# Kernel optimization log

Measured on AMD Instinct MI355X. Metric: run time of the kernel, lower is better.

The kernel has to match this reference:

```python
import jax, jax.numpy as jnp
import numpy as np

N_NODES = 20000
N_EDGES = 640000


def graph_conv(x, src, dst, W, b, n_nodes):
    """DGL GraphConv with norm='both': D_in^{-1/2} A D_out^{-1/2} X W + b."""
    ones = jnp.ones(src.shape[0], dtype=x.dtype)
    deg_out = jnp.maximum(jax.ops.segment_sum(ones, src, num_segments=n_nodes), 1.0)
    deg_in = jnp.maximum(jax.ops.segment_sum(ones, dst, num_segments=n_nodes), 1.0)
    xs = x * (deg_out ** -0.5)[:, None]          # scale src features
    agg = jax.ops.segment_sum(xs[src], dst, num_segments=n_nodes)  # [N, d]
    agg = agg * (deg_in ** -0.5)[:, None]
    return agg @ W + b


def setup_inputs() -> dict:
    key = jax.random.key(0)
    ks = jax.random.split(key, 10)
    d = 256
    scale = 1.0 / np.sqrt(d)
    return {
        "x": jax.random.normal(ks[0], (N_NODES, d), dtype=jnp.float32),
        "side_src": jax.random.randint(ks[1], (N_EDGES,), 0, N_NODES),
        "side_dst": jax.random.randint(ks[2], (N_EDGES,), 0, N_NODES),
        "upd_src": jax.random.randint(ks[3], (N_EDGES,), 0, N_NODES),
        "upd_dst": jax.random.randint(ks[4], (N_EDGES,), 0, N_NODES),
        "W1_side": jax.random.normal(ks[5], (d, d), dtype=jnp.float32) * scale,
        "b1_side": jnp.zeros((d,), dtype=jnp.float32),
        "W1_upd": jax.random.normal(ks[6], (d, d), dtype=jnp.float32) * scale,
        "b1_upd": jnp.zeros((d,), dtype=jnp.float32),
        "W2_side": jax.random.normal(ks[7], (d, d), dtype=jnp.float32) * scale,
        "b2_side": jnp.zeros((d,), dtype=jnp.float32),
        "W2_upd": jax.random.normal(ks[8], (d, d), dtype=jnp.float32) * scale,
        "b2_upd": jnp.zeros((d,), dtype=jnp.float32),
    }


def reference(x, side_src, side_dst, upd_src, upd_dst,
              W1_side, b1_side, W1_upd, b1_upd,
              W2_side, b2_side, W2_upd, b2_upd):
    n = x.shape[0]
    # layer 1: HeteroGraphConv with aggregate='sum' over relations, then relu
    h = (graph_conv(x, side_src, side_dst, W1_side, b1_side, n)
         + graph_conv(x, upd_src, upd_dst, W1_upd, b1_upd, n))
    h = jax.nn.relu(h)
    # layer 2
    out = (graph_conv(h, side_src, side_dst, W2_side, b2_side, n)
           + graph_conv(h, upd_src, upd_dst, W2_upd, b2_upd, n))
    return out
```

## Files before the change

### kernel.cpp

```cpp
#include <hip/hip_runtime.h>

typedef __attribute__((ext_vector_type(8))) short short8;
typedef __attribute__((ext_vector_type(4))) float f32x4;

#define SCHUNK 2048
#define MAXN   20480
#define NSLICE 8
#define NPB    40

__device__ inline unsigned short f2bf(float v) {
    unsigned u = __float_as_uint(v);
    u += 0x7FFFu + ((u >> 16) & 1u);
    return (unsigned short)(u >> 16);
}
__device__ inline float bf2f(unsigned short h) {
    return __uint_as_float((unsigned)h << 16);
}

__global__ void bias_sum_kernel(const float* __restrict__ b1s, const float* __restrict__ b1u,
                                const float* __restrict__ b2s, const float* __restrict__ b2u,
                                float* __restrict__ bsum1, float* __restrict__ bsum2) {
    int i = threadIdx.x;
    bsum1[i] = b1s[i] + b1u[i];
    bsum2[i] = b2s[i] + b2u[i];
}

__global__ void wprep_kernel(const float* __restrict__ W1s, const float* __restrict__ W1u,
                             const float* __restrict__ W2s, const float* __restrict__ W2u,
                             unsigned short* __restrict__ Bpk1, unsigned short* __restrict__ Bpk2) {
    int k = blockIdx.x;
    int nn = threadIdx.x;
    int layer = blockIdx.y;
    const float* Ws = layer ? W2s : W1s;
    const float* Wu = layer ? W2u : W1u;
    float w = (k < 256) ? Ws[k * 256 + nn] : Wu[(k - 256) * 256 + nn];
    unsigned short hi = f2bf(w);
    unsigned short lo = f2bf(w - bf2f(hi));
    unsigned short* B = layer ? Bpk2 : Bpk1;
    size_t frag = ((size_t)(nn >> 4) * 16 + (k >> 5)) * 2;
    size_t addr = frag * 512 + ((nn & 15) + ((k >> 3) & 3) * 16) * 8 + (k & 7);
    B[addr] = hi;
    B[addr + 512] = lo;
}

__global__ __launch_bounds__(256) void hist_kernel(
    const int* __restrict__ sS, const int* __restrict__ dS,
    const int* __restrict__ sU, const int* __restrict__ dU,
    int Es, int Eu, int n, int nblk, unsigned int* __restrict__ histG) {
    __shared__ unsigned int h[MAXN];
    const int rel = blockIdx.y;
    const int* src = rel ? sU : sS;
    const int* dst = rel ? dU : dS;
    int E = rel ? Eu : Es;
    int b = blockIdx.x;
    int chunk = (E + nblk - 1) / nblk;
    int beg = b * chunk;
    int end = min(E, beg + chunk);
    for (int i = threadIdx.x; i < n; i += 256) h[i] = 0u;
    __syncthreads();
    for (int i = beg + threadIdx.x; i < end; i += 256) {
        atomicAdd(&h[src[i]], 1u);
        atomicAdd(&h[dst[i]], 0x10000u);
    }
    __syncthreads();
    unsigned int* out = histG + ((size_t)rel * nblk + b) * n;
    for (int i = threadIdx.x; i < n; i += 256) out[i] = h[i];
}

__global__ void totals_kernel(const unsigned int* __restrict__ histG, int n, int nblk,
                              float* __restrict__ sOutS, float* __restrict__ sInS,
                              float* __restrict__ sOutU, float* __restrict__ sInU,
                              int* __restrict__ degInS, int* __restrict__ degInU) {
    const int rel = blockIdx.y;
    int i = blockIdx.x * 256 + threadIdx.x;
    if (i >= n) return;
    const unsigned int* hg = histG + (size_t)rel * nblk * n + i;
    unsigned int lo = 0, hi = 0;
    int b = 0;
    for (; b + 8 <= nblk; b += 8) {
        unsigned v0 = hg[(size_t)(b + 0) * n];
        unsigned v1 = hg[(size_t)(b + 1) * n];
        unsigned v2 = hg[(size_t)(b + 2) * n];
        unsigned v3 = hg[(size_t)(b + 3) * n];
        unsigned v4 = hg[(size_t)(b + 4) * n];
        unsigned v5 = hg[(size_t)(b + 5) * n];
        unsigned v6 = hg[(size_t)(b + 6) * n];
        unsigned v7 = hg[(size_t)(b + 7) * n];
        lo += (v0 & 0xFFFFu) + (v1 & 0xFFFFu) + (v2 & 0xFFFFu) + (v3 & 0xFFFFu)
            + (v4 & 0xFFFFu) + (v5 & 0xFFFFu) + (v6 & 0xFFFFu) + (v7 & 0xFFFFu);
        hi += (v0 >> 16) + (v1 >> 16) + (v2 >> 16) + (v3 >> 16)
            + (v4 >> 16) + (v5 >> 16) + (v6 >> 16) + (v7 >> 16);
    }
    for (; b < nblk; ++b) {
        unsigned v = hg[(size_t)b * n];
        lo += v & 0xFFFFu;
        hi += v >> 16;
    }
    float so = rsqrtf((float)(lo > 1u ? lo : 1u));
    float si = rsqrtf((float)(hi > 1u ? hi : 1u));
    if (rel) { sOutU[i] = so; sInU[i] = si; degInU[i] = (int)hi; }
    else     { sOutS[i] = so; sInS[i] = si; degInS[i] = (int)hi; }
}

__global__ __launch_bounds__(256) void scan_part_kernel(const int* __restrict__ degA,
                                                        const int* __restrict__ degB,
                                                        int n, int NB, int* __restrict__ bsum) {
    const int rel = blockIdx.y;
    const int* deg = rel ? degB : degA;
    int t = threadIdx.x;
    int base = blockIdx.x * SCHUNK + t * 8;
    int s = 0;
    if (base + 8 <= n) {
        int4 a = *(const int4*)(deg + base);
        int4 b = *(const int4*)(deg + base + 4);
        s = a.x + a.y + a.z + a.w + b.x + b.y + b.z + b.w;
    } else {
        for (int i = 0; i < 8; ++i)
            if (base + i < n) s += deg[base + i];
    }
    __shared__ int sm[256];
    sm[t] = s;
    __syncthreads();
    for (int off = 128; off > 0; off >>= 1) {
        if (t < off) sm[t] += sm[t + off];
        __syncthreads();
    }
    if (t == 0) bsum[rel * NB + blockIdx.x] = sm[0];
}

__global__ void scan_mid_kernel(int* __restrict__ bsum, int NB,
                                int* __restrict__ rpA, int* __restrict__ rpB, int n) {
    int t = threadIdx.x;
    if (t >= 2) return;
    int* bs = bsum + t * NB;
    int run = 0;
    for (int i = 0; i < NB; ++i) {
        int v = bs[i];
        bs[i] = run;
        run += v;
    }
    int* rp = t ? rpB : rpA;
    rp[n] = run;
}

__global__ __launch_bounds__(256) void scan_final_kernel(const int* __restrict__ degA,
                                                         const int* __restrict__ degB,
                                                         const int* __restrict__ bsum,
                                                         int n, int NB,
                                                         int* __restrict__ rpA,
                                                         int* __restrict__ rpB) {
    const int rel = blockIdx.y;
    const int* deg = rel ? degB : degA;
    int* rp = rel ? rpB : rpA;
    int t = threadIdx.x;
    int base = blockIdx.x * SCHUNK + t * 8;
    int v[8];
    if (base + 8 <= n) {
        int4 a = *(const int4*)(deg + base);
        int4 b = *(const int4*)(deg + base + 4);
        v[0] = a.x; v[1] = a.y; v[2] = a.z; v[3] = a.w;
        v[4] = b.x; v[5] = b.y; v[6] = b.z; v[7] = b.w;
    } else {
        for (int i = 0; i < 8; ++i) v[i] = (base + i < n) ? deg[base + i] : 0;
    }
    int s = 0;
    #pragma unroll
    for (int i = 0; i < 8; ++i) s += v[i];
    __shared__ int sm[256];
    sm[t] = s;
    __syncthreads();
    #pragma unroll
    for (int off = 1; off < 256; off <<= 1) {
        int y = (t >= off) ? sm[t - off] : 0;
        __syncthreads();
        sm[t] += y;
        __syncthreads();
    }
    int run = bsum[rel * NB + blockIdx.x] + sm[t] - s;
    #pragma unroll
    for (int i = 0; i < 8; ++i) {
        if (base + i < n) rp[base + i] = run;
        run += v[i];
    }
}

__global__ void offsets_kernel(const unsigned int* __restrict__ histG,
                               const int* __restrict__ rpS, const int* __restrict__ rpU,
                               int n, int nblk, int* __restrict__ offsG) {
    const int rel = blockIdx.y;
    int i = blockIdx.x * 256 + threadIdx.x;
    if (i >= n) return;
    const unsigned int* hg = histG + (size_t)rel * nblk * n + i;
    int* og = offsG + (size_t)rel * nblk * n + i;
    int run = (rel ? rpU : rpS)[i];
    int b = 0;
    for (; b + 8 <= nblk; b += 8) {
        unsigned v0 = hg[(size_t)(b + 0) * n];
        unsigned v1 = hg[(size_t)(b + 1) * n];
        unsigned v2 = hg[(size_t)(b + 2) * n];
        unsigned v3 = hg[(size_t)(b + 3) * n];
        unsigned v4 = hg[(size_t)(b + 4) * n];
        unsigned v5 = hg[(size_t)(b + 5) * n];
        unsigned v6 = hg[(size_t)(b + 6) * n];
        unsigned v7 = hg[(size_t)(b + 7) * n];
        og[(size_t)(b + 0) * n] = run; run += (int)(v0 >> 16);
        og[(size_t)(b + 1) * n] = run; run += (int)(v1 >> 16);
        og[(size_t)(b + 2) * n] = run; run += (int)(v2 >> 16);
        og[(size_t)(b + 3) * n] = run; run += (int)(v3 >> 16);
        og[(size_t)(b + 4) * n] = run; run += (int)(v4 >> 16);
        og[(size_t)(b + 5) * n] = run; run += (int)(v5 >> 16);
        og[(size_t)(b + 6) * n] = run; run += (int)(v6 >> 16);
        og[(size_t)(b + 7) * n] = run; run += (int)(v7 >> 16);
    }
    for (; b < nblk; ++b) {
        unsigned v = hg[(size_t)b * n];
        og[(size_t)b * n] = run;
        run += (int)(v >> 16);
    }
}

__global__ __launch_bounds__(256) void csr_scatter_kernel(
    const int* __restrict__ sS, const int* __restrict__ dS,
    const int* __restrict__ sU, const int* __restrict__ dU,
    int Es, int Eu, int n, int nblk, const int* __restrict__ offsG,
    const float* __restrict__ sOutS, const float* __restrict__ sOutU,
    int2* __restrict__ csrPS, int2* __restrict__ csrPU) {
    __shared__ int off[MAXN];
    const int rel = blockIdx.y;
    const int* src = rel ? sU : sS;
    const int* dst = rel ? dU : dS;
    const float* so = rel ? sOutU : sOutS;
    int2* csrP = rel ? csrPU : csrPS;
    int E = rel ? Eu : Es;
    int b = blockIdx.x;
    int chunk = (E + nblk - 1) / nblk;
    int beg = b * chunk;
    int end = min(E, beg + chunk);
    const int* og = offsG + ((size_t)rel * nblk + b) * n;
    for (int i = threadIdx.x; i < n; i += 256) off[i] = og[i];
    __syncthreads();
    for (int i = beg + threadIdx.x; i < end; i += 256) {
        int s = src[i];
        int pos = atomicAdd(&off[dst[i]], 1);
        csrP[pos] = make_int2(s, __float_as_int(so[s]));
    }
}

__global__ __launch_bounds__(256) void pull_slice_kernel(
    const float4* __restrict__ xin,
    const int2* __restrict__ csrPS, const int2* __restrict__ csrPU,
    const int* __restrict__ rpS, const int* __restrict__ rpU,
    const float* __restrict__ sinS, const float* __restrict__ sinU,
    unsigned short* __restrict__ aggPk, int n) {
    int bid = blockIdx.x;
    int slice = bid & (NSLICE - 1);
    int rest = bid >> 3;
    int rel = rest & 1;
    int chunk = rest >> 1;
    const int2* csrP = rel ? csrPU : csrPS;
    const int* rp = rel ? rpU : rpS;
    const float* sinv = rel ? sinU : sinS;

    int wave = threadIdx.x >> 6;
    int lane = threadIdx.x & 63;
    int sub = lane >> 3;
    int sl = lane & 7;
    int fbase = slice * 8 + sl;
    int kstepg = rel * 8 + slice;

    int start = chunk * NPB;
    int lim = min(n, start + NPB);
    for (int node = start + wave; node < lim; node += 4) {
        int beg = rp[node], end = rp[node + 1];
        float ax = 0.f, ay = 0.f, az = 0.f, aw = 0.f;
        for (int eb = beg; eb < end; eb += 64) {
            int cnt = end - eb;
            if (cnt > 64) cnt = 64;
            int myu = 0;
            float myw = 0.f;
            if (lane < cnt) {
                int2 p = csrP[eb + lane];
                myu = p.x;
                myw = __int_as_float(p.y);
            }
            int jmax = (cnt + 7) >> 3;
            int j = 0;
            for (; j + 4 <= jmax; j += 4) {
                int i0 = j * 8 + sub;
                int u0 = __shfl(myu, i0);
                int u1 = __shfl(myu, i0 + 8);
                int u2 = __shfl(myu, i0 + 16);
                int u3 = __shfl(myu, i0 + 24);
                float w0 = __shfl(myw, i0);
                float w1 = __shfl(myw, i0 + 8);
                float w2 = __shfl(myw, i0 + 16);
                float w3 = __shfl(myw, i0 + 24);
                float4 a0 = xin[(size_t)u0 * 64 + fbase];
                float4 a1 = xin[(size_t)u1 * 64 + fbase];
                float4 a2 = xin[(size_t)u2 * 64 + fbase];
                float4 a3 = xin[(size_t)u3 * 64 + fbase];
                ax += w0 * a0.x + w1 * a1.x + w2 * a2.x + w3 * a3.x;
                ay += w0 * a0.y + w1 * a1.y + w2 * a2.y + w3 * a3.y;
                az += w0 * a0.z + w1 * a1.z + w2 * a2.z + w3 * a3.z;
                aw += w0 * a0.w + w1 * a1.w + w2 * a2.w + w3 * a3.w;
            }
            for (; j < jmax; ++j) {
                int idx = j * 8 + sub;
                int u = __shfl(myu, idx);
                float w = __shfl(myw, idx);
                float4 a = xin[(size_t)u * 64 + fbase];
                ax += w * a.x; ay += w * a.y; az += w * a.z; aw += w * a.w;
            }
        }
        ax += __shfl_xor(ax, 8);  ax += __shfl_xor(ax, 16); ax += __shfl_xor(ax, 32);
        ay += __shfl_xor(ay, 8);  ay += __shfl_xor(ay, 16); ay += __shfl_xor(ay, 32);
        az += __shfl_xor(az, 8);  az += __shfl_xor(az, 16); az += __shfl_xor(az, 32);
        aw += __shfl_xor(aw, 8);  aw += __shfl_xor(aw, 16); aw += __shfl_xor(aw, 32);
        if (sub == 0) {
            float si = sinv[node];
            float vx = si * ax, vy = si * ay, vz = si * az, vw = si * aw;
            ushort4 hi4 = make_ushort4(f2bf(vx), f2bf(vy), f2bf(vz), f2bf(vw));
            ushort4 lo4 = make_ushort4(f2bf(vx - bf2f(hi4.x)), f2bf(vy - bf2f(hi4.y)),
                                       f2bf(vz - bf2f(hi4.z)), f2bf(vw - bf2f(hi4.w)));
            size_t frag = ((size_t)(node >> 4) * 16 + kstepg) * 2;
            size_t addr = frag * 512 + ((node & 15) + (sl >> 1) * 16) * 8 + (sl & 1) * 4;
            *(ushort4*)&aggPk[addr] = hi4;
            *(ushort4*)&aggPk[addr + 512] = lo4;
        }
    }
}

template <int RELU>
__global__ __launch_bounds__(512) void gemm_mfma_kernel(
    const short8* __restrict__ Apk, const short8* __restrict__ Bpk,
    const float* __restrict__ bias, float* __restrict__ C, int M) {
    __shared__ short8 lds[42][64];
    int tid = threadIdx.x;
    int lane = tid & 63;
    int wv = tid >> 6;
    int mt0 = blockIdx.x * 5;
    int m0 = blockIdx.x * 80;
    if (m0 >= M) return;
    int nt0 = wv * 2;
    int col0 = wv * 32;
    int frow = lane & 15;

    f32x4 acc[5][2];
    #pragma unroll
    for (int fr = 0; fr < 5; ++fr)
        #pragma unroll
        for (int fc = 0; fc < 2; ++fc)
            acc[fr][fc] = (f32x4){0.f, 0.f, 0.f, 0.f};

    for (int ks = 0; ks < 16; ++ks) {
        __syncthreads();
        #pragma unroll
        for (int r = 0; r < 6; ++r) {
            int s = r * 512 + tid;
            if (s < 2688) {
                int f = s >> 6, l = s & 63;
                if (f < 10) {
                    int fr = f >> 1, pl = f & 1;
                    lds[f][l] = Apk[((size_t)(mt0 + fr) * 16 + ks) * 128 + pl * 64 + l];
                } else {
                    int q = f - 10;
                    int nt = q >> 1, pl = q & 1;
                    lds[f][l] = Bpk[((size_t)nt * 16 + ks) * 128 + pl * 64 + l];
                }
            }
        }
        __syncthreads();
        short8 bh[2], bl[2];
        #pragma unroll
        for (int fc = 0; fc < 2; ++fc) {
            bh[fc] = lds[10 + (nt0 + fc) * 2 + 0][lane];
            bl[fc] = lds[10 + (nt0 + fc) * 2 + 1][lane];
        }
        #pragma unroll
        for (int fr = 0; fr < 5; ++fr) {
            short8 ah = lds[fr * 2 + 0][lane];
            short8 al = lds[fr * 2 + 1][lane];
            #pragma unroll
            for (int fc = 0; fc < 2; ++fc) {
                acc[fr][fc] = __builtin_amdgcn_mfma_f32_16x16x32_bf16(ah, bh[fc], acc[fr][fc], 0, 0, 0);
                acc[fr][fc] = __builtin_amdgcn_mfma_f32_16x16x32_bf16(al, bh[fc], acc[fr][fc], 0, 0, 0);
                acc[fr][fc] = __builtin_amdgcn_mfma_f32_16x16x32_bf16(ah, bl[fc], acc[fr][fc], 0, 0, 0);
            }
        }
    }

    #pragma unroll
    for (int fr = 0; fr < 5; ++fr)
        #pragma unroll
        for (int fc = 0; fc < 2; ++fc) {
            int c = col0 + fc * 16 + frow;
            float bc = bias[c];
            int rb = m0 + fr * 16 + (lane >> 4) * 4;
            #pragma unroll
            for (int j = 0; j < 4; ++j) {
                int r = rb + j;
                if (r < M) {
                    float v = acc[fr][fc][j] + bc;
                    if (RELU) v = fmaxf(v, 0.f);
                    C[(size_t)r * 256 + c] = v;
                }
            }
        }
}

extern "C" void kernel_launch(void* const* d_in, const int* in_sizes, int n_in,
                              void* d_out, int out_size, void* d_ws, size_t ws_size,
                              hipStream_t stream) {
    const float* x   = (const float*)d_in[0];
    const int* sS    = (const int*)d_in[1];
    const int* dS    = (const int*)d_in[2];
    const int* sU    = (const int*)d_in[3];
    const int* dU    = (const int*)d_in[4];
    const float* W1s = (const float*)d_in[5];
    const float* b1s = (const float*)d_in[6];
    const float* W1u = (const float*)d_in[7];
    const float* b1u = (const float*)d_in[8];
    const float* W2s = (const float*)d_in[9];
    const float* b2s = (const float*)d_in[10];
    const float* W2u = (const float*)d_in[11];
    const float* b2u = (const float*)d_in[12];
    float* out = (float*)d_out;

    const int n  = in_sizes[0] / 256;
    const int Es = in_sizes[1];
    const int Eu = in_sizes[3];
    const int NB = (n + SCHUNK - 1) / SCHUNK;
    const int gemmGrid = (n + 79) / 80;
    const size_t AGG_BYTES = (size_t)((n + 15) / 16 + 16) * 16 * 2 * 512 * 2;
    const size_t BPK_BYTES = (size_t)16 * 16 * 2 * 512 * 2;

    auto plan = [&](int nb) -> size_t {
        size_t t = 0;
        auto add = [&](size_t b) { t = (t + 255) & ~(size_t)255; t += b; };
        add((size_t)2 * nb * n * 4);
        add((size_t)2 * nb * n * 4);
        add((size_t)(n + 1) * 4); add((size_t)(n + 1) * 4);
        add((size_t)n * 4); add((size_t)n * 4); add((size_t)n * 4); add((size_t)n * 4);
        add((size_t)n * 4); add((size_t)n * 4);
        add(256 * 4); add(256 * 4);
        add((size_t)2 * NB * 4);
        add((size_t)Es * 8); add((size_t)Eu * 8);
        add(2 * BPK_BYTES);
        add(AGG_BYTES);
        add((size_t)n * 256 * 4);
        return t;
    };
    const int nblk = (plan(128) <= ws_size) ? 128 : 32;

    char* ws = (char*)d_ws;
    size_t off = 0;
    auto alloc = [&](size_t bytes) -> void* {
        off = (off + 255) & ~(size_t)255;
        void* p = ws + off;
        off += bytes;
        return p;
    };

    unsigned int* histG = (unsigned int*)alloc((size_t)2 * nblk * n * 4);
    int* offsG   = (int*)alloc((size_t)2 * nblk * n * 4);
    int* rpS     = (int*)alloc((size_t)(n + 1) * 4);
    int* rpU     = (int*)alloc((size_t)(n + 1) * 4);
    float* sOutS = (float*)alloc((size_t)n * 4);
    float* sInS  = (float*)alloc((size_t)n * 4);
    float* sOutU = (float*)alloc((size_t)n * 4);
    float* sInU  = (float*)alloc((size_t)n * 4);
    int* degInS  = (int*)alloc((size_t)n * 4);
    int* degInU  = (int*)alloc((size_t)n * 4);
    float* bsum1 = (float*)alloc(256 * 4);
    float* bsum2 = (float*)alloc(256 * 4);
    int* bsumBlk = (int*)alloc((size_t)2 * NB * 4);
    int2* csrPS  = (int2*)alloc((size_t)Es * 8);
    int2* csrPU  = (int2*)alloc((size_t)Eu * 8);
    unsigned short* Bpk1 = (unsigned short*)alloc(2 * BPK_BYTES);
    unsigned short* Bpk2 = Bpk1 + BPK_BYTES / 2;
    unsigned short* aggPk = (unsigned short*)alloc(AGG_BYTES);
    float* h     = (float*)alloc((size_t)n * 256 * 4);

    bias_sum_kernel<<<1, 256, 0, stream>>>(b1s, b1u, b2s, b2u, bsum1, bsum2);
    wprep_kernel<<<dim3(512, 2), 256, 0, stream>>>(W1s, W1u, W2s, W2u, Bpk1, Bpk2);
    dim3 hg(nblk, 2);
    hist_kernel<<<hg, 256, 0, stream>>>(sS, dS, sU, dU, Es, Eu, n, nblk, histG);
    dim3 tg((n + 255) / 256, 2);
    totals_kernel<<<tg, 256, 0, stream>>>(histG, n, nblk, sOutS, sInS, sOutU, sInU,
                                          degInS, degInU);
    dim3 sg(NB, 2);
    scan_part_kernel<<<sg, 256, 0, stream>>>(degInS, degInU, n, NB, bsumBlk);
    scan_mid_kernel<<<1, 64, 0, stream>>>(bsumBlk, NB, rpS, rpU, n);
    scan_final_kernel<<<sg, 256, 0, stream>>>(degInS, degInU, bsumBlk, n, NB, rpS, rpU);
    offsets_kernel<<<tg, 256, 0, stream>>>(histG, rpS, rpU, n, nblk, offsG);
    csr_scatter_kernel<<<hg, 256, 0, stream>>>(sS, dS, sU, dU, Es, Eu, n, nblk, offsG,
                                               sOutS, sOutU, csrPS, csrPU);

    int chunks = (n + NPB - 1) / NPB;
    int pullGrid = NSLICE * 2 * chunks;
    const float4* x4 = (const float4*)x;
    const float4* h4 = (const float4*)h;
    const short8* A8 = (const short8*)aggPk;
    const short8* B81 = (const short8*)Bpk1;
    const short8* B82 = (const short8*)Bpk2;

    pull_slice_kernel<<<pullGrid, 256, 0, stream>>>(x4, csrPS, csrPU, rpS, rpU,
                                                    sInS, sInU, aggPk, n);
    gemm_mfma_kernel<1><<<gemmGrid, 512, 0, stream>>>(A8, B81, bsum1, h, n);
    pull_slice_kernel<<<pullGrid, 256, 0, stream>>>(h4, csrPS, csrPU, rpS, rpU,
                                                    sInS, sInU, aggPk, n);
    gemm_mfma_kernel<0><<<gemmGrid, 512, 0, stream>>>(A8, B82, bsum2, out, n);
}
```

Measured before the change: 456.6 us.

## Prefetch next node's edges into LDS and double-buffer GEMM tiles

In the pull kernel, each wave now stages the first 64 edges of its node in LDS and prefetches the next node's row pointers and edges while the current node is being gathered. This replaces per-edge shuffles with LDS reads and hides index-load latency. The GEMM kernel switches to double-buffered LDS with register staging, so global loads for the next k-step overlap MFMA work and one barrier per step is removed. The cost is more registers and LDS per block, which may reduce occupancy.

```diff
diff --git a/kernel.cpp b/kernel.cpp
--- a/kernel.cpp
+++ b/kernel.cpp
@@ -252,6 +252,7 @@
     const int* __restrict__ rpS, const int* __restrict__ rpU,
     const float* __restrict__ sinS, const float* __restrict__ sinU,
     unsigned short* __restrict__ aggPk, int n) {
+    __shared__ int2 elds[4][64];
     int bid = blockIdx.x;
     int slice = bid & (NSLICE - 1);
     int rest = bid >> 3;
@@ -270,42 +271,67 @@
 
     int start = chunk * NPB;
     int lim = min(n, start + NPB);
-    for (int node = start + wave; node < lim; node += 4) {
-        int beg = rp[node], end = rp[node + 1];
+    int node = start + wave;
+    if (node >= lim) return;
+
+    int beg = rp[node], end = rp[node + 1];
+    {
+        int cnt = min(end - beg, 64);
+        int2 p = make_int2(0, 0);
+        if (lane < cnt) p = csrP[beg + lane];
+        elds[wave][lane] = p;
+    }
+    const int2* ebase = &elds[wave][sub];
+
+    while (node < lim) {
+        int next = node + 4;
+        int nbeg = 0, nend = 0;
+        int2 np = make_int2(0, 0);
+        if (next < lim) {
+            nbeg = rp[next];
+            nend = rp[next + 1];
+            int ncnt = min(nend - nbeg, 64);
+            if (lane < ncnt) np = csrP[nbeg + lane];
+        }
         float ax = 0.f, ay = 0.f, az = 0.f, aw = 0.f;
-        for (int eb = beg; eb < end; eb += 64) {
-            int cnt = end - eb;
-            if (cnt > 64) cnt = 64;
+        int cnt = min(end - beg, 64);
+        int jmax = (cnt + 7) >> 3;
+        int j = 0;
+        for (; j + 4 <= jmax; j += 4) {
+            int2 e0 = ebase[(j + 0) * 8];
+            int2 e1 = ebase[(j + 1) * 8];
+            int2 e2 = ebase[(j + 2) * 8];
+            int2 e3 = ebase[(j + 3) * 8];
+            float4 a0 = xin[(size_t)e0.x * 64 + fbase];
+            float4 a1 = xin[(size_t)e1.x * 64 + fbase];
+            float4 a2 = xin[(size_t)e2.x * 64 + fbase];
+            float4 a3 = xin[(size_t)e3.x * 64 + fbase];
+            float w0 = __int_as_float(e0.y), w1 = __int_as_float(e1.y);
+            float w2 = __int_as_float(e2.y), w3 = __int_as_float(e3.y);
+            ax += w0 * a0.x + w1 * a1.x + w2 * a2.x + w3 * a3.x;
+            ay += w0 * a0.y + w1 * a1.y + w2 * a2.y + w3 * a3.y;
+            az += w0 * a0.z + w1 * a1.z + w2 * a2.z + w3 * a3.z;
+            aw += w0 * a0.w + w1 * a1.w + w2 * a2.w + w3 * a3.w;
+        }
+        for (; j < jmax; ++j) {
+            int2 e = ebase[j * 8];
+            float4 a = xin[(size_t)e.x * 64 + fbase];
+            float w = __int_as_float(e.y);
+            ax += w * a.x; ay += w * a.y; az += w * a.z; aw += w * a.w;
+        }
+        for (int eb = beg + 64; eb < end; eb += 64) {
+            int scnt = end - eb;
+            if (scnt > 64) scnt = 64;
             int myu = 0;
             float myw = 0.f;
-            if (lane < cnt) {
+            if (lane < scnt) {
                 int2 p = csrP[eb + lane];
                 myu = p.x;
                 myw = __int_as_float(p.y);
             }
-            int jmax = (cnt + 7) >> 3;
-            int j = 0;
-            for (; j + 4 <= jmax; j += 4) {
-                int i0 = j * 8 + sub;
-                int u0 = __shfl(myu, i0);
-                int u1 = __shfl(myu, i0 + 8);
-                int u2 = __shfl(myu, i0 + 16);
-                int u3 = __shfl(myu, i0 + 24);
-                float w0 = __shfl(myw, i0);
-                float w1 = __shfl(myw, i0 + 8);
-                float w2 = __shfl(myw, i0 + 16);
-                float w3 = __shfl(myw, i0 + 24);
-                float4 a0 = xin[(size_t)u0 * 64 + fbase];
-                float4 a1 = xin[(size_t)u1 * 64 + fbase];
-                float4 a2 = xin[(size_t)u2 * 64 + fbase];
-                float4 a3 = xin[(size_t)u3 * 64 + fbase];
-                ax += w0 * a0.x + w1 * a1.x + w2 * a2.x + w3 * a3.x;
-                ay += w0 * a0.y + w1 * a1.y + w2 * a2.y + w3 * a3.y;
-                az += w0 * a0.z + w1 * a1.z + w2 * a2.z + w3 * a3.z;
-                aw += w0 * a0.w + w1 * a1.w + w2 * a2.w + w3 * a3.w;
-            }
-            for (; j < jmax; ++j) {
-                int idx = j * 8 + sub;
+            int sjmax = (scnt + 7) >> 3;
+            for (int sj = 0; sj < sjmax; ++sj) {
+                int idx = sj * 8 + sub;
                 int u = __shfl(myu, idx);
                 float w = __shfl(myw, idx);
                 float4 a = xin[(size_t)u * 64 + fbase];
@@ -327,6 +353,10 @@
             *(ushort4*)&aggPk[addr] = hi4;
             *(ushort4*)&aggPk[addr + 512] = lo4;
         }
+        if (next < lim) elds[wave][lane] = np;
+        beg = nbeg;
+        end = nend;
+        node = next;
     }
 }
 
@@ -334,7 +364,7 @@
 __global__ __launch_bounds__(512) void gemm_mfma_kernel(
     const short8* __restrict__ Apk, const short8* __restrict__ Bpk,
     const float* __restrict__ bias, float* __restrict__ C, int M) {
-    __shared__ short8 lds[42][64];
+    __shared__ short8 lds[2][42][64];
     int tid = threadIdx.x;
     int lane = tid & 63;
     int wv = tid >> 6;
@@ -345,6 +375,24 @@
     int col0 = wv * 32;
     int frow = lane & 15;
 
+    int sf[6], sln[6];
+    bool sv[6];
+    #pragma unroll
+    for (int r = 0; r < 6; ++r) {
+        int s = r * 512 + tid;
+        sv[r] = s < 2688;
+        sf[r] = s >> 6;
+        sln[r] = s & 63;
+    }
+    auto gaddr = [&](int f, int l, int ks) -> size_t {
+        if (f < 10) {
+            return ((size_t)(mt0 + (f >> 1)) * 16 + ks) * 128 + (f & 1) * 64 + l;
+        } else {
+            int q = f - 10;
+            return ((size_t)(q >> 1) * 16 + ks) * 128 + (q & 1) * 64 + l;
+        }
+    };
+
     f32x4 acc[5][2];
     #pragma unroll
     for (int fr = 0; fr < 5; ++fr)
@@ -352,40 +400,45 @@
         for (int fc = 0; fc < 2; ++fc)
             acc[fr][fc] = (f32x4){0.f, 0.f, 0.f, 0.f};
 
+    short8 stg[6];
+    #pragma unroll
+    for (int r = 0; r < 6; ++r)
+        if (sv[r]) stg[r] = (sf[r] < 10 ? Apk : Bpk)[gaddr(sf[r], sln[r], 0)];
+    #pragma unroll
+    for (int r = 0; r < 6; ++r)
+        if (sv[r]) lds[0][sf[r]][sln[r]] = stg[r];
+    __syncthreads();
+
+    int cur = 0;
     for (int ks = 0; ks < 16; ++ks) {
-        __syncthreads();
-        #pragma unroll
-        for (int r = 0; r < 6; ++r) {
-            int s = r * 512 + tid;
-            if (s < 2688) {
-                int f = s >> 6, l = s & 63;
-                if (f < 10) {
-                    int fr = f >> 1, pl = f & 1;
-                    lds[f][l] = Apk[((size_t)(mt0 + fr) * 16 + ks) * 128 + pl * 64 + l];
-                } else {
-                    int q = f - 10;
-                    int nt = q >> 1, pl = q & 1;
-                    lds[f][l] = Bpk[((size_t)nt * 16 + ks) * 128 + pl * 64 + l];
-                }
-            }
-        }
-        __syncthreads();
+        if (ks + 1 < 16) {
+            #pragma unroll
+            for (int r = 0; r < 6; ++r)
+                if (sv[r]) stg[r] = (sf[r] < 10 ? Apk : Bpk)[gaddr(sf[r], sln[r], ks + 1)];
+        }
         short8 bh[2], bl[2];
         #pragma unroll
         for (int fc = 0; fc < 2; ++fc) {
-            bh[fc] = lds[10 + (nt0 + fc) * 2 + 0][lane];
-            bl[fc] = lds[10 + (nt0 + fc) * 2 + 1][lane];
+            bh[fc] = lds[cur][10 + (nt0 + fc) * 2 + 0][lane];
+            bl[fc] = lds[cur][10 + (nt0 + fc) * 2 + 1][lane];
         }
         #pragma unroll
         for (int fr = 0; fr < 5; ++fr) {
-            short8 ah = lds[fr * 2 + 0][lane];
-            short8 al = lds[fr * 2 + 1][lane];
+            short8 ah = lds[cur][fr * 2 + 0][lane];
+            short8 al = lds[cur][fr * 2 + 1][lane];
             #pragma unroll
             for (int fc = 0; fc < 2; ++fc) {
                 acc[fr][fc] = __builtin_amdgcn_mfma_f32_16x16x32_bf16(ah, bh[fc], acc[fr][fc], 0, 0, 0);
                 acc[fr][fc] = __builtin_amdgcn_mfma_f32_16x16x32_bf16(al, bh[fc], acc[fr][fc], 0, 0, 0);
                 acc[fr][fc] = __builtin_amdgcn_mfma_f32_16x16x32_bf16(ah, bl[fc], acc[fr][fc], 0, 0, 0);
             }
+        }
+        if (ks + 1 < 16) {
+            #pragma unroll
+            for (int r = 0; r < 6; ++r)
+                if (sv[r]) lds[cur ^ 1][sf[r]][sln[r]] = stg[r];
+            __syncthreads();
+            cur ^= 1;
         }
     }
 
```

Measured after the change: 457.2 us. About the same (+0.1%).
